# Performance work log

Measured on AMD Instinct MI355X. Metric: run time of the kernel, lower is better.

The kernel has to match this reference:

```python
import jax, jax.numpy as jnp
import numpy as np

H = 8  # number of heads


def setup_inputs() -> dict:
    key = jax.random.key(0)
    ks = jax.random.split(key, 5)
    B, L, D = 4, 2048, 512
    scale = 1.0 / np.sqrt(D)
    return {
        "query": jax.random.normal(ks[0], (B, L, D), dtype=jnp.float32),
        "keys": jax.random.normal(ks[1], (B, L, D), dtype=jnp.float32),
        "Wq": jax.random.normal(ks[2], (D, D), dtype=jnp.float32) * scale,
        "Wk": jax.random.normal(ks[3], (D, D), dtype=jnp.float32) * scale,
        "Wv": jax.random.normal(ks[4], (D, D), dtype=jnp.float32) * scale,
    }


def reference(query, keys, Wq, Wk, Wv):
    B, Lq, D = query.shape
    Lk = keys.shape[1]
    dh = D // H
    # Linear layers (torch nn.Linear: y = x @ W.T), then split heads.
    Q = (query @ Wq.T).reshape(B, Lq, H, dh)
    K = (keys @ Wk.T).reshape(B, Lk, H, dh)
    V = (keys @ Wv.T).reshape(B, Lk, H, dh)
    # NOTE: original scales by sqrt(key_dim) == sqrt(D), not sqrt(head_dim).
    inv_scale = 1.0 / jnp.sqrt(jnp.float32(D))
    scores = jnp.einsum("bqhd,bkhd->bhqk", Q, K) * inv_scale  # [B,H,Lq,Lk]
    attn = jax.nn.softmax(scores, axis=-1)
    # dropout_p = 0 (eval); no dropout applied.
    out = jnp.einsum("bhqk,bkhd->bqhd", attn, V).reshape(B, Lq, D)
    return out + query  # residual
```

## Files before the change

kernel.cpp:

```cpp
#include <hip/hip_runtime.h>

typedef unsigned short u16;
typedef unsigned int   u32;
typedef short  s16x8  __attribute__((ext_vector_type(8)));
typedef float  f32x16 __attribute__((ext_vector_type(16)));

__device__ __forceinline__ u16 f2bf(float f) {
    union { u32 i; float f; } x; x.f = f;
    u32 r = x.i + 0x7fffu + ((x.i >> 16) & 1u);
    return (u16)(r >> 16);
}

#define PD 512

__global__ __launch_bounds__(256) void proj_mfma(
    const float* __restrict__ query, const float* __restrict__ keys,
    const float* __restrict__ Wq, const float* __restrict__ Wk, const float* __restrict__ Wv,
    u16* __restrict__ Qo, u16* __restrict__ Ko, u16* __restrict__ Vt)
{
    const int z = blockIdx.z;
    const float* __restrict__ X = (z == 0) ? query : keys;
    const float* __restrict__ W = (z == 0) ? Wq : ((z == 1) ? Wk : Wv);
    const int bx = blockIdx.x;
    const int by = blockIdx.y;

    const float* __restrict__ Amat = (z < 2) ? X : W;
    const float* __restrict__ Bmat = (z < 2) ? W : X;
    const int a0 = ((z < 2) ? bx : by) * 128;
    const int b0 = ((z < 2) ? by : bx) * 128;

    __shared__ u16 As[128][40];
    __shared__ u16 Bs[128][40];

    const int tid  = threadIdx.x;
    const int wave = tid >> 6, lane = tid & 63;
    const int wm = wave >> 1, wn = wave & 1;
    const int l31 = lane & 31, lh = lane >> 5;

    const int srow = tid >> 1;
    const int sk   = (tid & 1) * 16;

    f32x16 acc[2][2];
    #pragma unroll
    for (int i = 0; i < 2; ++i)
        #pragma unroll
        for (int j = 0; j < 2; ++j)
            #pragma unroll
            for (int r = 0; r < 16; ++r) acc[i][j][r] = 0.f;

    for (int k0 = 0; k0 < PD; k0 += 32) {
        __syncthreads();
        {
            const float* ap = Amat + (size_t)(a0 + srow) * PD + k0 + sk;
            const float* bp = Bmat + (size_t)(b0 + srow) * PD + k0 + sk;
            u16 ab[16], bb[16];
            #pragma unroll
            for (int i = 0; i < 16; i += 4) {
                float4 av = *(const float4*)(ap + i);
                float4 bv = *(const float4*)(bp + i);
                ab[i+0] = f2bf(av.x); ab[i+1] = f2bf(av.y); ab[i+2] = f2bf(av.z); ab[i+3] = f2bf(av.w);
                bb[i+0] = f2bf(bv.x); bb[i+1] = f2bf(bv.y); bb[i+2] = f2bf(bv.z); bb[i+3] = f2bf(bv.w);
            }
            *(uint4*)&As[srow][sk]     = *(uint4*)&ab[0];
            *(uint4*)&As[srow][sk + 8] = *(uint4*)&ab[8];
            *(uint4*)&Bs[srow][sk]     = *(uint4*)&bb[0];
            *(uint4*)&Bs[srow][sk + 8] = *(uint4*)&bb[8];
        }
        __syncthreads();

        #pragma unroll
        for (int ks = 0; ks < 2; ++ks) {
            s16x8 af[2], bfr[2];
            #pragma unroll
            for (int mf = 0; mf < 2; ++mf) {
                uint4 v = *(uint4*)&As[wm*64 + mf*32 + l31][ks*16 + lh*8];
                af[mf] = *(s16x8*)&v;
            }
            #pragma unroll
            for (int nf = 0; nf < 2; ++nf) {
                uint4 v = *(uint4*)&Bs[wn*64 + nf*32 + l31][ks*16 + lh*8];
                bfr[nf] = *(s16x8*)&v;
            }
            #pragma unroll
            for (int mf = 0; mf < 2; ++mf)
                #pragma unroll
                for (int nf = 0; nf < 2; ++nf)
                    acc[mf][nf] = __builtin_amdgcn_mfma_f32_32x32x16_bf16(
                        af[mf], bfr[nf], acc[mf][nf], 0, 0, 0);
        }
    }

    const float osc = (z == 0) ? 0.044194173824159216f : 1.0f;
    u16* __restrict__ O = (z == 0) ? Qo : Ko;
    #pragma unroll
    for (int mf = 0; mf < 2; ++mf)
        #pragma unroll
        for (int nf = 0; nf < 2; ++nf)
            #pragma unroll
            for (int r = 0; r < 16; ++r) {
                const int mi = a0 + wm*64 + mf*32 + (r & 3) + 8*(r >> 2) + 4*lh;
                const int ni = b0 + wn*64 + nf*32 + l31;
                const u16 v = f2bf(acc[mf][nf][r] * osc);
                if (z < 2) {
                    O[(size_t)mi * PD + ni] = v;
                } else {
                    const int bb_ = ni >> 11, ll = ni & 2047;
                    Vt[((size_t)(bb_ * 512 + mi)) * 2048 + ll] = v;
                }
            }
}

__global__ __launch_bounds__(256) void attn_mfma(
    const u16* __restrict__ Qp, const u16* __restrict__ Kp, const u16* __restrict__ Vt,
    const float* __restrict__ query, float* __restrict__ out)
{
    const int qt = blockIdx.x;
    const int h  = blockIdx.y;
    const int b  = blockIdx.z;
    const int q0 = qt * 128;
    const int L = 2048;

    __shared__ uint4 lds_u4[36864 / 16];
    u16* Ks   = (u16*)lds_u4;
    u16* Vts  = Ks + 64 * 72;
    u16* P2a  = Vts + 64 * 72;
    float* Oe = (float*)lds_u4;

    const int tid  = threadIdx.x;
    const int wave = tid >> 6, lane = tid & 63;
    const int l31 = lane & 31, lh = lane >> 5;
    u16* P2 = P2a + wave * 32 * 72;

    const int qrow = b * L + q0 + wave * 32 + l31;
    s16x8 qf[4];
    #pragma unroll
    for (int ds = 0; ds < 4; ++ds) {
        uint4 v = *(const uint4*)(Qp + (size_t)qrow * PD + h*64 + ds*16 + lh*8);
        qf[ds] = *(s16x8*)&v;
    }

    f32x16 ot[2];
    #pragma unroll
    for (int mf = 0; mf < 2; ++mf)
        #pragma unroll
        for (int r = 0; r < 16; ++r) ot[mf][r] = 0.f;
    float m_i = -INFINITY, l_i = 0.f;

    const int srow = tid >> 2;
    const int sc   = (tid & 3) * 16;

    for (int k0 = 0; k0 < L; k0 += 64) {
        __syncthreads();
        {
            const u16* kp = Kp + (size_t)(b*L + k0 + srow) * PD + h*64 + sc;
            const u16* vp = Vt + ((size_t)((b*8 + h)*64 + srow)) * 2048 + k0 + sc;
            uint4 k0v = *(const uint4*)kp;
            uint4 k1v = *(const uint4*)(kp + 8);
            uint4 v0v = *(const uint4*)vp;
            uint4 v1v = *(const uint4*)(vp + 8);
            *(uint4*)&Ks [srow*72 + sc]     = k0v;
            *(uint4*)&Ks [srow*72 + sc + 8] = k1v;
            *(uint4*)&Vts[srow*72 + sc]     = v0v;
            *(uint4*)&Vts[srow*72 + sc + 8] = v1v;
        }
        __syncthreads();

        f32x16 s[2];
        #pragma unroll
        for (int kf = 0; kf < 2; ++kf) {
            #pragma unroll
            for (int r = 0; r < 16; ++r) s[kf][r] = 0.f;
            #pragma unroll
            for (int ds = 0; ds < 4; ++ds) {
                uint4 av = *(uint4*)&Ks[(kf*32 + l31)*72 + ds*16 + lh*8];
                s[kf] = __builtin_amdgcn_mfma_f32_32x32x16_bf16(
                    *(s16x8*)&av, qf[ds], s[kf], 0, 0, 0);
            }
        }

        float rm = -INFINITY;
        #pragma unroll
        for (int kf = 0; kf < 2; ++kf)
            #pragma unroll
            for (int r = 0; r < 16; ++r) rm = fmaxf(rm, s[kf][r]);
        rm = fmaxf(rm, __shfl_xor(rm, 32));
        const float m_new = fmaxf(m_i, rm);
        const float alpha = __expf(m_i - m_new);
        float rs = 0.f;
        u16 pb[2][16];
        #pragma unroll
        for (int kf = 0; kf < 2; ++kf)
            #pragma unroll
            for (int r = 0; r < 16; ++r) {
                const float p = __expf(s[kf][r] - m_new);
                rs += p;
                pb[kf][r] = f2bf(p);
            }
        rs += __shfl_xor(rs, 32);
        l_i = l_i * alpha + rs;
        m_i = m_new;
        #pragma unroll
        for (int mf = 0; mf < 2; ++mf)
            #pragma unroll
            for (int r = 0; r < 16; ++r) ot[mf][r] *= alpha;

        #pragma unroll
        for (int kf = 0; kf < 2; ++kf)
            #pragma unroll
            for (int g = 0; g < 4; ++g) {
                const u32 lo = (u32)pb[kf][g*4+0] | ((u32)pb[kf][g*4+1] << 16);
                const u32 hi = (u32)pb[kf][g*4+2] | ((u32)pb[kf][g*4+3] << 16);
                uint2 w2; w2.x = lo; w2.y = hi;
                *(uint2*)&P2[l31*72 + kf*32 + g*8 + lh*4] = w2;
            }

        #pragma unroll
        for (int ks = 0; ks < 4; ++ks) {
            uint4 bv = *(uint4*)&P2[l31*72 + ks*16 + lh*8];
            s16x8 bfr = *(s16x8*)&bv;
            #pragma unroll
            for (int mf = 0; mf < 2; ++mf) {
                uint4 av = *(uint4*)&Vts[(mf*32 + l31)*72 + ks*16 + lh*8];
                ot[mf] = __builtin_amdgcn_mfma_f32_32x32x16_bf16(
                    *(s16x8*)&av, bfr, ot[mf], 0, 0, 0);
            }
        }
    }

    __syncthreads();
    const float inv_l = 1.0f / l_i;
    #pragma unroll
    for (int mf = 0; mf < 2; ++mf)
        #pragma unroll
        for (int g = 0; g < 4; ++g) {
            float4 v;
            v.x = ot[mf][g*4+0] * inv_l;
            v.y = ot[mf][g*4+1] * inv_l;
            v.z = ot[mf][g*4+2] * inv_l;
            v.w = ot[mf][g*4+3] * inv_l;
            const int dh0 = mf*32 + 8*g + 4*lh;
            *(float4*)&Oe[(wave*32 + l31)*68 + dh0] = v;
        }
    __syncthreads();
    {
        const int r  = tid >> 1;
        const int c0 = (tid & 1) * 32;
        const size_t gb = ((size_t)(b*L + q0 + r)) * PD + h*64 + c0;
        #pragma unroll
        for (int i = 0; i < 8; ++i) {
            float4 ov = *(float4*)&Oe[r*68 + c0 + 4*i];
            float4 qv = *(const float4*)(query + gb + 4*i);
            ov.x += qv.x; ov.y += qv.y; ov.z += qv.z; ov.w += qv.w;
            *(float4*)(out + gb + 4*i) = ov;
        }
    }
}

extern "C" void kernel_launch(void* const* d_in, const int* in_sizes, int n_in,
                              void* d_out, int out_size, void* d_ws, size_t ws_size,
                              hipStream_t stream) {
    const float* query = (const float*)d_in[0];
    const float* keys  = (const float*)d_in[1];
    const float* Wq    = (const float*)d_in[2];
    const float* Wk    = (const float*)d_in[3];
    const float* Wv    = (const float*)d_in[4];
    float* out = (float*)d_out;

    u16* Qp = (u16*)d_ws;
    u16* Kp = Qp + (size_t)8192 * 512;
    u16* Vt = Kp + (size_t)8192 * 512;

    proj_mfma<<<dim3(64, 4, 3), 256, 0, stream>>>(query, keys, Wq, Wk, Wv, Qp, Kp, Vt);
    attn_mfma<<<dim3(16, 8, 4), 256, 0, stream>>>(Qp, Kp, Vt, query, out);
}
```

Measured before the change: 188.9 us.

## Keep P in registers via cross-lane shuffles, use exp2 with folded log2e

The attention kernel no longer writes the softmax probabilities to shared memory and reads them back as MFMA operands. Lanes now exchange packed bf16 pairs with __shfl_xor so the B fragment is built directly in registers. The log2(e) factor is folded into the Q projection scale so the softmax can use exp2f instead of __expf. Float-to-bf16 conversion switches to the packed hip_bf16 intrinsic, which may map to a hardware conversion instruction. Together these remove LDS round trips and conversion ALU work in the inner loop, at the cost of extra cross-lane shuffle traffic.

```diff
diff --git a/kernel.cpp b/kernel.cpp
--- a/kernel.cpp
+++ b/kernel.cpp
@@ -1,4 +1,5 @@
 #include <hip/hip_runtime.h>
+#include <hip/hip_bf16.h>
 
 typedef unsigned short u16;
 typedef unsigned int   u32;
@@ -9,6 +10,10 @@
     union { u32 i; float f; } x; x.f = f;
     u32 r = x.i + 0x7fffu + ((x.i >> 16) & 1u);
     return (u16)(r >> 16);
+}
+__device__ __forceinline__ u32 pk_bf16(float a, float b) {
+    __hip_bfloat162 h = __float22bfloat162_rn(make_float2(a, b));
+    union { __hip_bfloat162 h; u32 u; } c; c.h = h; return c.u;
 }
 
 #define PD 512
@@ -53,18 +58,20 @@
         {
             const float* ap = Amat + (size_t)(a0 + srow) * PD + k0 + sk;
             const float* bp = Bmat + (size_t)(b0 + srow) * PD + k0 + sk;
-            u16 ab[16], bb[16];
-            #pragma unroll
-            for (int i = 0; i < 16; i += 4) {
-                float4 av = *(const float4*)(ap + i);
-                float4 bv = *(const float4*)(bp + i);
-                ab[i+0] = f2bf(av.x); ab[i+1] = f2bf(av.y); ab[i+2] = f2bf(av.z); ab[i+3] = f2bf(av.w);
-                bb[i+0] = f2bf(bv.x); bb[i+1] = f2bf(bv.y); bb[i+2] = f2bf(bv.z); bb[i+3] = f2bf(bv.w);
-            }
-            *(uint4*)&As[srow][sk]     = *(uint4*)&ab[0];
-            *(uint4*)&As[srow][sk + 8] = *(uint4*)&ab[8];
-            *(uint4*)&Bs[srow][sk]     = *(uint4*)&bb[0];
-            *(uint4*)&Bs[srow][sk + 8] = *(uint4*)&bb[8];
+            u32 aw[8], bw[8];
+            #pragma unroll
+            for (int i = 0; i < 4; ++i) {
+                float4 av = *(const float4*)(ap + 4*i);
+                float4 bv = *(const float4*)(bp + 4*i);
+                aw[2*i]   = pk_bf16(av.x, av.y);
+                aw[2*i+1] = pk_bf16(av.z, av.w);
+                bw[2*i]   = pk_bf16(bv.x, bv.y);
+                bw[2*i+1] = pk_bf16(bv.z, bv.w);
+            }
+            *(uint4*)&As[srow][sk]     = *(uint4*)&aw[0];
+            *(uint4*)&As[srow][sk + 8] = *(uint4*)&aw[4];
+            *(uint4*)&Bs[srow][sk]     = *(uint4*)&bw[0];
+            *(uint4*)&Bs[srow][sk + 8] = *(uint4*)&bw[4];
         }
         __syncthreads();
 
@@ -90,7 +97,7 @@
         }
     }
 
-    const float osc = (z == 0) ? 0.044194173824159216f : 1.0f;
+    const float osc = (z == 0) ? (0.044194173824159216f * 1.4426950408889634f) : 1.0f;
     u16* __restrict__ O = (z == 0) ? Qo : Ko;
     #pragma unroll
     for (int mf = 0; mf < 2; ++mf)
@@ -123,13 +130,11 @@
     __shared__ uint4 lds_u4[36864 / 16];
     u16* Ks   = (u16*)lds_u4;
     u16* Vts  = Ks + 64 * 72;
-    u16* P2a  = Vts + 64 * 72;
     float* Oe = (float*)lds_u4;
 
     const int tid  = threadIdx.x;
     const int wave = tid >> 6, lane = tid & 63;
     const int l31 = lane & 31, lh = lane >> 5;
-    u16* P2 = P2a + wave * 32 * 72;
 
     const int qrow = b * L + q0 + wave * 32 + l31;
     s16x8 qf[4];
@@ -185,16 +190,20 @@
             for (int r = 0; r < 16; ++r) rm = fmaxf(rm, s[kf][r]);
         rm = fmaxf(rm, __shfl_xor(rm, 32));
         const float m_new = fmaxf(m_i, rm);
-        const float alpha = __expf(m_i - m_new);
+        const float alpha = exp2f(m_i - m_new);
         float rs = 0.f;
-        u16 pb[2][16];
+        u32 pq[2][4][2];
         #pragma unroll
         for (int kf = 0; kf < 2; ++kf)
             #pragma unroll
-            for (int r = 0; r < 16; ++r) {
-                const float p = __expf(s[kf][r] - m_new);
-                rs += p;
-                pb[kf][r] = f2bf(p);
+            for (int g = 0; g < 4; ++g) {
+                float p0 = exp2f(s[kf][4*g+0] - m_new);
+                float p1 = exp2f(s[kf][4*g+1] - m_new);
+                float p2 = exp2f(s[kf][4*g+2] - m_new);
+                float p3 = exp2f(s[kf][4*g+3] - m_new);
+                rs += (p0 + p1) + (p2 + p3);
+                pq[kf][g][0] = pk_bf16(p0, p1);
+                pq[kf][g][1] = pk_bf16(p2, p3);
             }
         rs += __shfl_xor(rs, 32);
         l_i = l_i * alpha + rs;
@@ -207,24 +216,24 @@
         #pragma unroll
         for (int kf = 0; kf < 2; ++kf)
             #pragma unroll
-            for (int g = 0; g < 4; ++g) {
-                const u32 lo = (u32)pb[kf][g*4+0] | ((u32)pb[kf][g*4+1] << 16);
-                const u32 hi = (u32)pb[kf][g*4+2] | ((u32)pb[kf][g*4+3] << 16);
-                uint2 w2; w2.x = lo; w2.y = hi;
-                *(uint2*)&P2[l31*72 + kf*32 + g*8 + lh*4] = w2;
-            }
-
-        #pragma unroll
-        for (int ks = 0; ks < 4; ++ks) {
-            uint4 bv = *(uint4*)&P2[l31*72 + ks*16 + lh*8];
-            s16x8 bfr = *(s16x8*)&bv;
-            #pragma unroll
-            for (int mf = 0; mf < 2; ++mf) {
-                uint4 av = *(uint4*)&Vts[(mf*32 + l31)*72 + ks*16 + lh*8];
-                ot[mf] = __builtin_amdgcn_mfma_f32_32x32x16_bf16(
-                    *(s16x8*)&av, bfr, ot[mf], 0, 0, 0);
-            }
-        }
+            for (int t = 0; t < 2; ++t) {
+                const int g_own  = 2*t + lh;
+                const int g_send = 2*t + (lh ^ 1);
+                const u32 sx = __shfl_xor((int)pq[kf][g_send][0], 32);
+                const u32 sy = __shfl_xor((int)pq[kf][g_send][1], 32);
+                const u32 ox = pq[kf][g_own][0], oy = pq[kf][g_own][1];
+                union { u32 w[4]; s16x8 v; } bu;
+                bu.w[0] = lh ? sx : ox;
+                bu.w[1] = lh ? sy : oy;
+                bu.w[2] = lh ? ox : sx;
+                bu.w[3] = lh ? oy : sy;
+                #pragma unroll
+                for (int mf = 0; mf < 2; ++mf) {
+                    uint4 av = *(uint4*)&Vts[(mf*32 + l31)*72 + kf*32 + t*16 + lh*8];
+                    ot[mf] = __builtin_amdgcn_mfma_f32_32x32x16_bf16(
+                        *(s16x8*)&av, bu.v, ot[mf], 0, 0, 0);
+                }
+            }
     }
 
     __syncthreads();
```

Result: slower. 244.7 us (+29.5%).
